# Kernel optimization log

Hardware: AMD Instinct MI355X
Metric: run time of the kernel (lower is better)

The kernel has to match this reference:

```python
import jax, jax.numpy as jnp
import numpy as np

B, S, I, H, O = 32, 64, 256, 256, 128


def setup_inputs() -> dict:
    key = jax.random.key(0)
    ks = jax.random.split(key, 8)
    init_k = 1.0 / np.sqrt(H)
    F = H + I
    return {
        "sentence": jax.random.normal(ks[0], (B, S, I), dtype=jnp.float32),
        "weight": jax.random.uniform(ks[1], (H, F), minval=-init_k, maxval=init_k, dtype=jnp.float32),
        "weight_lambda": jax.random.uniform(ks[2], (H, F), minval=0.0, maxval=1.0, dtype=jnp.float32),
        "weight_gamma": jax.random.uniform(ks[3], (H, F), minval=-0.001 * init_k, maxval=0.001 * init_k, dtype=jnp.float32),
        "bias": jax.random.uniform(ks[4], (H,), minval=-init_k, maxval=init_k, dtype=jnp.float32),
        "out_w": jax.random.uniform(ks[5], (O, H), minval=-init_k, maxval=init_k, dtype=jnp.float32),
        "out_b": jax.random.uniform(ks[6], (O,), minval=-init_k, maxval=init_k, dtype=jnp.float32),
    }


def reference(sentence, weight, weight_lambda, weight_gamma, bias, out_w, out_b):
    b, s, i = sentence.shape
    h_dim = weight.shape[0]
    f_dim = weight.shape[1]  # h_dim + i
    h0 = jnp.zeros((b, h_dim), dtype=sentence.dtype)
    f0 = jnp.zeros((b, h_dim, f_dim), dtype=sentence.dtype)

    def step(carry, x_t):
        h, f = carry
        total_input = jnp.concatenate([x_t, h], axis=1)          # (b, f_dim)
        total_weights = weight + f                                # (b, h, f_dim)
        pre = jnp.einsum('bf,bhf->bh', total_input, total_weights)
        norm = jnp.sqrt(jnp.sum(total_weights * total_weights, axis=2)) + 1e-16  # (b, h)
        h_new = jnp.tanh(pre / norm + bias)
        f_new = weight_lambda * (f / norm[..., None]) + \
                weight_gamma * jnp.einsum('bh,bf->bhf', h_new, total_input)
        return (h_new, f_new), None

    (h_fin, f_fin), _ = jax.lax.scan(step, (h0, f0), jnp.swapaxes(sentence, 0, 1))
    tag_space = h_fin @ out_w.T + out_b
    return tag_space, h_fin, f_fin
```

## Files before the change

### kernel.cpp

```cpp
#include <hip/hip_runtime.h>

#define Bq 32
#define Sq 64
#define Iq 256
#define Hq 256
#define Oq 128
#define Fq 512
#define WPB 8
#define NT 512

__global__ __launch_bounds__(NT, 2) void stpn_main(
    const float* __restrict__ x,
    const float* __restrict__ w,
    const float* __restrict__ wl,
    const float* __restrict__ wgm,
    const float* __restrict__ bias,
    float* __restrict__ out,
    unsigned long long* __restrict__ hb)
{
    const int blk   = blockIdx.x;
    const int b     = blk & 31;
    const int chunk = blk >> 5;
    const int h0    = chunk * 32;
    const int tid   = threadIdx.x;
    const int lr    = tid & 15;
    const int r     = tid >> 4;
    const int row   = h0 + r;

    __shared__ float ti[2][Fq];

    float fw[32], fl[32], fg[32], ff[32];
    const size_t rowoff = (size_t)row * Fq;
#pragma unroll
    for (int j = 0; j < 8; ++j) {
        const int c = 4 * lr + 64 * j;
        const float4 a = *(const float4*)(w   + rowoff + c);
        const float4 l = *(const float4*)(wl  + rowoff + c);
        const float4 g = *(const float4*)(wgm + rowoff + c);
        fw[4*j+0]=a.x; fw[4*j+1]=a.y; fw[4*j+2]=a.z; fw[4*j+3]=a.w;
        fl[4*j+0]=l.x; fl[4*j+1]=l.y; fl[4*j+2]=l.z; fl[4*j+3]=l.w;
        fg[4*j+0]=g.x; fg[4*j+1]=g.y; fg[4*j+2]=g.z; fg[4*j+3]=g.w;
    }
#pragma unroll
    for (int j = 0; j < 32; ++j) ff[j] = 0.f;

    const float brow = bias[row];
    const float* xb = x + (size_t)b * Sq * Iq;

    for (int t = 0; t < Sq; ++t) {
        const int p = t & 1;
        if (tid < Iq) {
            ti[p][tid] = xb[(size_t)t * Iq + tid];
        } else {
            const int hh = tid - Iq;
            float hv = 0.f;
            if (t > 0) {
                unsigned long long* slot =
                    hb + (size_t)((t - 1) & 1) * Bq * Hq + (size_t)b * Hq + hh;
                unsigned long long v;
                for (;;) {
                    v = __hip_atomic_load(slot, __ATOMIC_RELAXED,
                                          __HIP_MEMORY_SCOPE_AGENT);
                    if ((unsigned)(v >> 32) == (unsigned)t) break;
                }
                hv = __uint_as_float((unsigned)(v & 0xffffffffu));
            }
            ti[p][Iq + hh] = hv;
        }
        __syncthreads();

        float pre = 0.f, nsq = 0.f;
#pragma unroll
        for (int j = 0; j < 8; ++j) {
            const float4 tv = *(const float4*)&ti[p][4 * lr + 64 * j];
            float tw;
            tw = fw[4*j+0] + ff[4*j+0]; pre = fmaf(tv.x, tw, pre); nsq = fmaf(tw, tw, nsq);
            tw = fw[4*j+1] + ff[4*j+1]; pre = fmaf(tv.y, tw, pre); nsq = fmaf(tw, tw, nsq);
            tw = fw[4*j+2] + ff[4*j+2]; pre = fmaf(tv.z, tw, pre); nsq = fmaf(tw, tw, nsq);
            tw = fw[4*j+3] + ff[4*j+3]; pre = fmaf(tv.w, tw, pre); nsq = fmaf(tw, tw, nsq);
        }
#pragma unroll
        for (int m = 1; m < 16; m <<= 1) {
            pre += __shfl_xor(pre, m, 16);
            nsq += __shfl_xor(nsq, m, 16);
        }
        const float inv = 1.f / (sqrtf(nsq) + 1e-16f);
        const float hn  = tanhf(fmaf(pre, inv, brow));

        if (lr == 0) {
            if (t < Sq - 1) {
                const unsigned long long pk =
                    ((unsigned long long)(unsigned)(t + 1) << 32) |
                    (unsigned long long)__float_as_uint(hn);
                __hip_atomic_store(
                    hb + (size_t)(t & 1) * Bq * Hq + (size_t)b * Hq + row, pk,
                    __ATOMIC_RELAXED, __HIP_MEMORY_SCOPE_AGENT);
            } else {
                out[Bq * Oq + (size_t)b * Hq + row] = hn;
            }
        }

#pragma unroll
        for (int j = 0; j < 8; ++j) {
            const float4 tv = *(const float4*)&ti[p][4 * lr + 64 * j];
            ff[4*j+0] = fmaf(fl[4*j+0], ff[4*j+0] * inv, fg[4*j+0] * (hn * tv.x));
            ff[4*j+1] = fmaf(fl[4*j+1], ff[4*j+1] * inv, fg[4*j+1] * (hn * tv.y));
            ff[4*j+2] = fmaf(fl[4*j+2], ff[4*j+2] * inv, fg[4*j+2] * (hn * tv.z));
            ff[4*j+3] = fmaf(fl[4*j+3], ff[4*j+3] * inv, fg[4*j+3] * (hn * tv.w));
        }
    }

    float* fo = out + Bq * Oq + Bq * Hq + (size_t)b * Hq * Fq + rowoff;
#pragma unroll
    for (int j = 0; j < 8; ++j) {
        const int c = 4 * lr + 64 * j;
        float4 v;
        v.x = ff[4*j+0]; v.y = ff[4*j+1]; v.z = ff[4*j+2]; v.w = ff[4*j+3];
        *(float4*)(fo + c) = v;
    }
}

__global__ void stpn_tag(const float* __restrict__ ow, const float* __restrict__ ob,
                         float* out)
{
    const int b = blockIdx.x;
    const int o = threadIdx.x;
    const float* hf = out + Bq * Oq + (size_t)b * Hq;
    const float* wr = ow + (size_t)o * Hq;
    float acc = ob[o];
#pragma unroll 8
    for (int h = 0; h < Hq; ++h) acc = fmaf(hf[h], wr[h], acc);
    out[b * Oq + o] = acc;
}

extern "C" void kernel_launch(void* const* d_in, const int* in_sizes, int n_in,
                              void* d_out, int out_size, void* d_ws, size_t ws_size,
                              hipStream_t stream)
{
    const float* x    = (const float*)d_in[0];
    const float* w    = (const float*)d_in[1];
    const float* wl   = (const float*)d_in[2];
    const float* wgm  = (const float*)d_in[3];
    const float* bias = (const float*)d_in[4];
    const float* ow   = (const float*)d_in[5];
    const float* ob   = (const float*)d_in[6];
    float* out = (float*)d_out;

    hipMemsetAsync(d_ws, 0, 2 * Bq * Hq * sizeof(unsigned long long), stream);

    stpn_main<<<Bq * WPB, NT, 0, stream>>>(x, w, wl, wgm, bias, out,
                                           (unsigned long long*)d_ws);
    stpn_tag<<<Bq, Oq, 0, stream>>>(ow, ob, out);
}
```

Measured before the change: 161.0 us.

## Move norm and x-part of recurrence off the critical path, local h reuse

Restructures the per-timestep loop so that the weight norm and the input-part dot product for step t+1 are computed right after the plastic-weight update, leaving only the h-part dot product between the cross-block h exchange and tanh. It also writes the block's own h rows to shared memory and skips spinning on them, splits x and h into separate double-buffered shared arrays with x prefetched two steps ahead, and uses a fast exp-based tanh and a fast divide. The tag kernel becomes a 16-lane shuffle-reduced GEMV. The fast tanh and fast divide slightly change numerics, and there is extra register pressure from the tw_h and xv arrays.

After: 198.6 us. 1.23x slower.

```diff
diff --git a/kernel.cpp b/kernel.cpp
--- a/kernel.cpp
+++ b/kernel.cpp
@@ -8,6 +8,11 @@
 #define Fq 512
 #define WPB 8
 #define NT 512
+
+__device__ __forceinline__ float fast_tanh(float v) {
+    const float e = __expf(2.0f * v);
+    return 1.0f - __fdividef(2.0f, e + 1.0f);
+}
 
 __global__ __launch_bounds__(NT, 2) void stpn_main(
     const float* __restrict__ x,
@@ -27,19 +32,17 @@
     const int r     = tid >> 4;
     const int row   = h0 + r;
 
-    __shared__ float ti[2][Fq];
+    __shared__ float xls[2][Iq];
+    __shared__ float hls[2][Hq];
 
     float fw[32], fl[32], fg[32], ff[32];
     const size_t rowoff = (size_t)row * Fq;
 #pragma unroll
     for (int j = 0; j < 8; ++j) {
         const int c = 4 * lr + 64 * j;
-        const float4 a = *(const float4*)(w   + rowoff + c);
-        const float4 l = *(const float4*)(wl  + rowoff + c);
-        const float4 g = *(const float4*)(wgm + rowoff + c);
-        fw[4*j+0]=a.x; fw[4*j+1]=a.y; fw[4*j+2]=a.z; fw[4*j+3]=a.w;
-        fl[4*j+0]=l.x; fl[4*j+1]=l.y; fl[4*j+2]=l.z; fl[4*j+3]=l.w;
-        fg[4*j+0]=g.x; fg[4*j+1]=g.y; fg[4*j+2]=g.z; fg[4*j+3]=g.w;
+        *(float4*)&fw[4*j] = *(const float4*)(w   + rowoff + c);
+        *(float4*)&fl[4*j] = *(const float4*)(wl  + rowoff + c);
+        *(float4*)&fg[4*j] = *(const float4*)(wgm + rowoff + c);
     }
 #pragma unroll
     for (int j = 0; j < 32; ++j) ff[j] = 0.f;
@@ -47,48 +50,78 @@
     const float brow = bias[row];
     const float* xb = x + (size_t)b * Sq * Iq;
 
+    float xr = 0.f;
+    if (tid < Iq) {
+        xls[0][tid] = xb[tid];
+        xr = xb[Iq + tid];
+    }
+    __syncthreads();
+
+    float tw_h[16];
+    float xv[16];
+    float nsq = 0.f, xpre = 0.f;
+#pragma unroll
+    for (int j = 0; j < 4; ++j) {
+        const float4 x4 = *(const float4*)&xls[0][4 * lr + 64 * j];
+        *(float4*)&xv[4*j] = x4;
+        float tw;
+        tw = fw[4*j+0]; nsq = fmaf(tw, tw, nsq); xpre = fmaf(x4.x, tw, xpre);
+        tw = fw[4*j+1]; nsq = fmaf(tw, tw, nsq); xpre = fmaf(x4.y, tw, xpre);
+        tw = fw[4*j+2]; nsq = fmaf(tw, tw, nsq); xpre = fmaf(x4.z, tw, xpre);
+        tw = fw[4*j+3]; nsq = fmaf(tw, tw, nsq); xpre = fmaf(x4.w, tw, xpre);
+    }
+#pragma unroll
+    for (int j = 0; j < 16; ++j) {
+        const float tw = fw[16 + j];
+        tw_h[j] = tw; nsq = fmaf(tw, tw, nsq);
+    }
+#pragma unroll
+    for (int m = 1; m < 16; m <<= 1) nsq += __shfl_xor(nsq, m, 16);
+    float inv = __fdividef(1.0f, sqrtf(nsq) + 1e-16f);
+
     for (int t = 0; t < Sq; ++t) {
-        const int p = t & 1;
+        const int pp = (t - 1) & 1;
         if (tid < Iq) {
-            ti[p][tid] = xb[(size_t)t * Iq + tid];
+            if (t + 1 < Sq) xls[(t + 1) & 1][tid] = xr;
+            if (t + 2 < Sq) xr = xb[(size_t)(t + 2) * Iq + tid];
         } else {
             const int hh = tid - Iq;
-            float hv = 0.f;
-            if (t > 0) {
+            if (t > 0 && (hh < h0 || hh >= h0 + 32)) {
                 unsigned long long* slot =
-                    hb + (size_t)((t - 1) & 1) * Bq * Hq + (size_t)b * Hq + hh;
+                    hb + (size_t)pp * Bq * Hq + (size_t)b * Hq + hh;
                 unsigned long long v;
-                for (;;) {
+                do {
                     v = __hip_atomic_load(slot, __ATOMIC_RELAXED,
                                           __HIP_MEMORY_SCOPE_AGENT);
-                    if ((unsigned)(v >> 32) == (unsigned)t) break;
-                }
-                hv = __uint_as_float((unsigned)(v & 0xffffffffu));
-            }
-            ti[p][Iq + hh] = hv;
+                } while ((unsigned)(v >> 32) != (unsigned)t);
+                hls[pp][hh] = __uint_as_float((unsigned)(v & 0xffffffffu));
+            }
         }
         __syncthreads();
 
-        float pre = 0.f, nsq = 0.f;
-#pragma unroll
-        for (int j = 0; j < 8; ++j) {
-            const float4 tv = *(const float4*)&ti[p][4 * lr + 64 * j];
-            float tw;
-            tw = fw[4*j+0] + ff[4*j+0]; pre = fmaf(tv.x, tw, pre); nsq = fmaf(tw, tw, nsq);
-            tw = fw[4*j+1] + ff[4*j+1]; pre = fmaf(tv.y, tw, pre); nsq = fmaf(tw, tw, nsq);
-            tw = fw[4*j+2] + ff[4*j+2]; pre = fmaf(tv.z, tw, pre); nsq = fmaf(tw, tw, nsq);
-            tw = fw[4*j+3] + ff[4*j+3]; pre = fmaf(tv.w, tw, pre); nsq = fmaf(tw, tw, nsq);
-        }
-#pragma unroll
-        for (int m = 1; m < 16; m <<= 1) {
-            pre += __shfl_xor(pre, m, 16);
-            nsq += __shfl_xor(nsq, m, 16);
-        }
-        const float inv = 1.f / (sqrtf(nsq) + 1e-16f);
-        const float hn  = tanhf(fmaf(pre, inv, brow));
+        float hv[16];
+        float pre = xpre;
+        if (t > 0) {
+#pragma unroll
+            for (int j = 0; j < 4; ++j) {
+                const float4 h4 = *(const float4*)&hls[pp][4 * lr + 64 * j];
+                *(float4*)&hv[4*j] = h4;
+                pre = fmaf(h4.x, tw_h[4*j+0], pre);
+                pre = fmaf(h4.y, tw_h[4*j+1], pre);
+                pre = fmaf(h4.z, tw_h[4*j+2], pre);
+                pre = fmaf(h4.w, tw_h[4*j+3], pre);
+            }
+        } else {
+#pragma unroll
+            for (int j = 0; j < 16; ++j) hv[j] = 0.f;
+        }
+#pragma unroll
+        for (int m = 1; m < 16; m <<= 1) pre += __shfl_xor(pre, m, 16);
+        const float hn = fast_tanh(fmaf(pre, inv, brow));
 
         if (lr == 0) {
             if (t < Sq - 1) {
+                hls[t & 1][row] = hn;
                 const unsigned long long pk =
                     ((unsigned long long)(unsigned)(t + 1) << 32) |
                     (unsigned long long)__float_as_uint(hn);
@@ -101,12 +134,33 @@
         }
 
 #pragma unroll
-        for (int j = 0; j < 8; ++j) {
-            const float4 tv = *(const float4*)&ti[p][4 * lr + 64 * j];
-            ff[4*j+0] = fmaf(fl[4*j+0], ff[4*j+0] * inv, fg[4*j+0] * (hn * tv.x));
-            ff[4*j+1] = fmaf(fl[4*j+1], ff[4*j+1] * inv, fg[4*j+1] * (hn * tv.y));
-            ff[4*j+2] = fmaf(fl[4*j+2], ff[4*j+2] * inv, fg[4*j+2] * (hn * tv.z));
-            ff[4*j+3] = fmaf(fl[4*j+3], ff[4*j+3] * inv, fg[4*j+3] * (hn * tv.w));
+        for (int j = 0; j < 16; ++j)
+            ff[j] = fmaf(fl[j], ff[j] * inv, fg[j] * (hn * xv[j]));
+#pragma unroll
+        for (int j = 0; j < 16; ++j)
+            ff[16+j] = fmaf(fl[16+j], ff[16+j] * inv, fg[16+j] * (hn * hv[j]));
+
+        if (t < Sq - 1) {
+            const int q = (t + 1) & 1;
+            nsq = 0.f; xpre = 0.f;
+#pragma unroll
+            for (int j = 0; j < 4; ++j) {
+                const float4 x4 = *(const float4*)&xls[q][4 * lr + 64 * j];
+                *(float4*)&xv[4*j] = x4;
+                float tw;
+                tw = fw[4*j+0] + ff[4*j+0]; nsq = fmaf(tw, tw, nsq); xpre = fmaf(x4.x, tw, xpre);
+                tw = fw[4*j+1] + ff[4*j+1]; nsq = fmaf(tw, tw, nsq); xpre = fmaf(x4.y, tw, xpre);
+                tw = fw[4*j+2] + ff[4*j+2]; nsq = fmaf(tw, tw, nsq); xpre = fmaf(x4.z, tw, xpre);
+                tw = fw[4*j+3] + ff[4*j+3]; nsq = fmaf(tw, tw, nsq); xpre = fmaf(x4.w, tw, xpre);
+            }
+#pragma unroll
+            for (int j = 0; j < 16; ++j) {
+                const float tw = fw[16+j] + ff[16+j];
+                tw_h[j] = tw; nsq = fmaf(tw, tw, nsq);
+            }
+#pragma unroll
+            for (int m = 1; m < 16; m <<= 1) nsq += __shfl_xor(nsq, m, 16);
+            inv = __fdividef(1.0f, sqrtf(nsq) + 1e-16f);
         }
     }
 
@@ -114,23 +168,39 @@
 #pragma unroll
     for (int j = 0; j < 8; ++j) {
         const int c = 4 * lr + 64 * j;
-        float4 v;
-        v.x = ff[4*j+0]; v.y = ff[4*j+1]; v.z = ff[4*j+2]; v.w = ff[4*j+3];
-        *(float4*)(fo + c) = v;
-    }
-}
-
-__global__ void stpn_tag(const float* __restrict__ ow, const float* __restrict__ ob,
-                         float* out)
+        *(float4*)(fo + c) = *(const float4*)&ff[4*j];
+    }
+}
+
+__global__ __launch_bounds__(256) void stpn_tag(
+    const float* __restrict__ ow, const float* __restrict__ ob,
+    float* __restrict__ out)
 {
-    const int b = blockIdx.x;
-    const int o = threadIdx.x;
-    const float* hf = out + Bq * Oq + (size_t)b * Hq;
-    const float* wr = ow + (size_t)o * Hq;
-    float acc = ob[o];
-#pragma unroll 8
-    for (int h = 0; h < Hq; ++h) acc = fmaf(hf[h], wr[h], acc);
-    out[b * Oq + o] = acc;
+    const int b   = blockIdx.x;
+    const int tid = threadIdx.x;
+    const int l   = tid & 15;
+    const int g   = tid >> 4;
+    const float* hf = out + Bq * Oq + (size_t)b * Hq + l * 16;
+    const float4 h0 = ((const float4*)hf)[0];
+    const float4 h1 = ((const float4*)hf)[1];
+    const float4 h2 = ((const float4*)hf)[2];
+    const float4 h3 = ((const float4*)hf)[3];
+#pragma unroll
+    for (int p = 0; p < 8; ++p) {
+        const int o = g * 8 + p;
+        const float* wr = ow + (size_t)o * Hq + l * 16;
+        const float4 w0 = ((const float4*)wr)[0];
+        const float4 w1 = ((const float4*)wr)[1];
+        const float4 w2 = ((const float4*)wr)[2];
+        const float4 w3 = ((const float4*)wr)[3];
+        float acc = h0.x*w0.x + h0.y*w0.y + h0.z*w0.z + h0.w*w0.w
+                  + h1.x*w1.x + h1.y*w1.y + h1.z*w1.z + h1.w*w1.w
+                  + h2.x*w2.x + h2.y*w2.y + h2.z*w2.z + h2.w*w2.w
+                  + h3.x*w3.x + h3.y*w3.y + h3.z*w3.z + h3.w*w3.w;
+#pragma unroll
+        for (int m = 1; m < 16; m <<= 1) acc += __shfl_xor(acc, m, 16);
+        if (l == 0) out[b * Oq + o] = acc + ob[o];
+    }
 }
 
 extern "C" void kernel_launch(void* const* d_in, const int* in_sizes, int n_in,
@@ -150,5 +220,5 @@
 
     stpn_main<<<Bq * WPB, NT, 0, stream>>>(x, w, wl, wgm, bias, out,
                                            (unsigned long long*)d_ws);
-    stpn_tag<<<Bq, Oq, 0, stream>>>(ow, ob, out);
-}
+    stpn_tag<<<Bq, 256, 0, stream>>>(ow, ob, out);
+}
```

## Move norm computation off critical path, fuse tag projection, use fast tanh

Applied to the files above, without the earlier changes.

Each row's norm of weight+f is now computed after the f update, so it is ready before the next step's h exchange. That takes the squared-norm reduction and its shuffles off the latency-critical path between publishing h and the next step. tanhf is replaced by an exp-based fast approximation. The separate output-projection kernel is folded into chunk-0 blocks, which spin-wait on the final h values, removing one kernel launch. The fast tanh gives slightly different rounding, and the fused tail adds serial work to a few blocks.

Result: slower. 182.2 us (+13.2%).

```diff
diff --git a/kernel.cpp b/kernel.cpp
--- a/kernel.cpp
+++ b/kernel.cpp
@@ -9,12 +9,19 @@
 #define WPB 8
 #define NT 512
 
+__device__ __forceinline__ float fast_tanh(float v) {
+    const float e = __expf(2.0f * v);
+    return 1.0f - __fdividef(2.0f, e + 1.0f);
+}
+
 __global__ __launch_bounds__(NT, 2) void stpn_main(
     const float* __restrict__ x,
     const float* __restrict__ w,
     const float* __restrict__ wl,
     const float* __restrict__ wgm,
     const float* __restrict__ bias,
+    const float* __restrict__ ow,
+    const float* __restrict__ ob,
     float* __restrict__ out,
     unsigned long long* __restrict__ hb)
 {
@@ -34,18 +41,22 @@
 #pragma unroll
     for (int j = 0; j < 8; ++j) {
         const int c = 4 * lr + 64 * j;
-        const float4 a = *(const float4*)(w   + rowoff + c);
-        const float4 l = *(const float4*)(wl  + rowoff + c);
-        const float4 g = *(const float4*)(wgm + rowoff + c);
-        fw[4*j+0]=a.x; fw[4*j+1]=a.y; fw[4*j+2]=a.z; fw[4*j+3]=a.w;
-        fl[4*j+0]=l.x; fl[4*j+1]=l.y; fl[4*j+2]=l.z; fl[4*j+3]=l.w;
-        fg[4*j+0]=g.x; fg[4*j+1]=g.y; fg[4*j+2]=g.z; fg[4*j+3]=g.w;
+        *(float4*)&fw[4*j] = *(const float4*)(w   + rowoff + c);
+        *(float4*)&fl[4*j] = *(const float4*)(wl  + rowoff + c);
+        *(float4*)&fg[4*j] = *(const float4*)(wgm + rowoff + c);
     }
 #pragma unroll
     for (int j = 0; j < 32; ++j) ff[j] = 0.f;
 
     const float brow = bias[row];
     const float* xb = x + (size_t)b * Sq * Iq;
+
+    float nsq = 0.f;
+#pragma unroll
+    for (int j = 0; j < 32; ++j) nsq = fmaf(fw[j], fw[j], nsq);
+#pragma unroll
+    for (int m = 1; m < 16; m <<= 1) nsq += __shfl_xor(nsq, m, 16);
+    float inv = __fdividef(1.0f, sqrtf(nsq) + 1e-16f);
 
     for (int t = 0; t < Sq; ++t) {
         const int p = t & 1;
@@ -58,46 +69,36 @@
                 unsigned long long* slot =
                     hb + (size_t)((t - 1) & 1) * Bq * Hq + (size_t)b * Hq + hh;
                 unsigned long long v;
-                for (;;) {
+                do {
                     v = __hip_atomic_load(slot, __ATOMIC_RELAXED,
                                           __HIP_MEMORY_SCOPE_AGENT);
-                    if ((unsigned)(v >> 32) == (unsigned)t) break;
-                }
+                } while ((unsigned)(v >> 32) != (unsigned)t);
                 hv = __uint_as_float((unsigned)(v & 0xffffffffu));
             }
             ti[p][Iq + hh] = hv;
         }
         __syncthreads();
 
-        float pre = 0.f, nsq = 0.f;
+        float pre = 0.f;
 #pragma unroll
         for (int j = 0; j < 8; ++j) {
             const float4 tv = *(const float4*)&ti[p][4 * lr + 64 * j];
-            float tw;
-            tw = fw[4*j+0] + ff[4*j+0]; pre = fmaf(tv.x, tw, pre); nsq = fmaf(tw, tw, nsq);
-            tw = fw[4*j+1] + ff[4*j+1]; pre = fmaf(tv.y, tw, pre); nsq = fmaf(tw, tw, nsq);
-            tw = fw[4*j+2] + ff[4*j+2]; pre = fmaf(tv.z, tw, pre); nsq = fmaf(tw, tw, nsq);
-            tw = fw[4*j+3] + ff[4*j+3]; pre = fmaf(tv.w, tw, pre); nsq = fmaf(tw, tw, nsq);
+            pre = fmaf(tv.x, fw[4*j+0] + ff[4*j+0], pre);
+            pre = fmaf(tv.y, fw[4*j+1] + ff[4*j+1], pre);
+            pre = fmaf(tv.z, fw[4*j+2] + ff[4*j+2], pre);
+            pre = fmaf(tv.w, fw[4*j+3] + ff[4*j+3], pre);
         }
 #pragma unroll
-        for (int m = 1; m < 16; m <<= 1) {
-            pre += __shfl_xor(pre, m, 16);
-            nsq += __shfl_xor(nsq, m, 16);
-        }
-        const float inv = 1.f / (sqrtf(nsq) + 1e-16f);
-        const float hn  = tanhf(fmaf(pre, inv, brow));
+        for (int m = 1; m < 16; m <<= 1) pre += __shfl_xor(pre, m, 16);
+        const float hn = fast_tanh(fmaf(pre, inv, brow));
 
         if (lr == 0) {
-            if (t < Sq - 1) {
-                const unsigned long long pk =
-                    ((unsigned long long)(unsigned)(t + 1) << 32) |
-                    (unsigned long long)__float_as_uint(hn);
-                __hip_atomic_store(
-                    hb + (size_t)(t & 1) * Bq * Hq + (size_t)b * Hq + row, pk,
-                    __ATOMIC_RELAXED, __HIP_MEMORY_SCOPE_AGENT);
-            } else {
-                out[Bq * Oq + (size_t)b * Hq + row] = hn;
-            }
+            const unsigned long long pk =
+                ((unsigned long long)(unsigned)(t + 1) << 32) |
+                (unsigned long long)__float_as_uint(hn);
+            __hip_atomic_store(
+                hb + (size_t)p * Bq * Hq + (size_t)b * Hq + row, pk,
+                __ATOMIC_RELAXED, __HIP_MEMORY_SCOPE_AGENT);
         }
 
 #pragma unroll
@@ -108,29 +109,54 @@
             ff[4*j+2] = fmaf(fl[4*j+2], ff[4*j+2] * inv, fg[4*j+2] * (hn * tv.z));
             ff[4*j+3] = fmaf(fl[4*j+3], ff[4*j+3] * inv, fg[4*j+3] * (hn * tv.w));
         }
+        if (t < Sq - 1) {
+            nsq = 0.f;
+#pragma unroll
+            for (int j = 0; j < 32; ++j) {
+                const float tw = fw[j] + ff[j];
+                nsq = fmaf(tw, tw, nsq);
+            }
+#pragma unroll
+            for (int m = 1; m < 16; m <<= 1) nsq += __shfl_xor(nsq, m, 16);
+            inv = __fdividef(1.0f, sqrtf(nsq) + 1e-16f);
+        }
     }
 
     float* fo = out + Bq * Oq + Bq * Hq + (size_t)b * Hq * Fq + rowoff;
 #pragma unroll
     for (int j = 0; j < 8; ++j) {
         const int c = 4 * lr + 64 * j;
-        float4 v;
-        v.x = ff[4*j+0]; v.y = ff[4*j+1]; v.z = ff[4*j+2]; v.w = ff[4*j+3];
-        *(float4*)(fo + c) = v;
+        *(float4*)(fo + c) = *(const float4*)&ff[4*j];
     }
-}
 
-__global__ void stpn_tag(const float* __restrict__ ow, const float* __restrict__ ob,
-                         float* out)
-{
-    const int b = blockIdx.x;
-    const int o = threadIdx.x;
-    const float* hf = out + Bq * Oq + (size_t)b * Hq;
-    const float* wr = ow + (size_t)o * Hq;
-    float acc = ob[o];
-#pragma unroll 8
-    for (int h = 0; h < Hq; ++h) acc = fmaf(hf[h], wr[h], acc);
-    out[b * Oq + o] = acc;
+    if (chunk == 0) {
+        if (tid < Hq) {
+            unsigned long long* slot =
+                hb + (size_t)1 * Bq * Hq + (size_t)b * Hq + tid;
+            unsigned long long v;
+            do {
+                v = __hip_atomic_load(slot, __ATOMIC_RELAXED,
+                                      __HIP_MEMORY_SCOPE_AGENT);
+            } while ((unsigned)(v >> 32) != (unsigned)Sq);
+            const float hv = __uint_as_float((unsigned)(v & 0xffffffffu));
+            ti[0][tid] = hv;
+            out[Bq * Oq + (size_t)b * Hq + tid] = hv;
+        }
+        __syncthreads();
+        const int o = tid >> 2;
+        const int l = tid & 3;
+        const float* wr = ow + (size_t)o * Hq + l * 64;
+        float acc = 0.f;
+#pragma unroll
+        for (int k = 0; k < 16; ++k) {
+            const float4 w4 = ((const float4*)wr)[k];
+            const float4 h4 = *(const float4*)&ti[0][l * 64 + 4 * k];
+            acc += w4.x * h4.x + w4.y * h4.y + w4.z * h4.z + w4.w * h4.w;
+        }
+        acc += __shfl_xor(acc, 1, 4);
+        acc += __shfl_xor(acc, 2, 4);
+        if (l == 0) out[(size_t)b * Oq + o] = acc + ob[o];
+    }
 }
 
 extern "C" void kernel_launch(void* const* d_in, const int* in_sizes, int n_in,
@@ -148,7 +174,6 @@
 
     hipMemsetAsync(d_ws, 0, 2 * Bq * Hq * sizeof(unsigned long long), stream);
 
-    stpn_main<<<Bq * WPB, NT, 0, stream>>>(x, w, wl, wgm, bias, out,
+    stpn_main<<<Bq * WPB, NT, 0, stream>>>(x, w, wl, wgm, bias, ow, ob, out,
                                            (unsigned long long*)d_ws);
-    stpn_tag<<<Bq, Oq, 0, stream>>>(ow, ob, out);
 }
```
